# Kernel tuning notes

Measured on AMD Instinct MI355X. Metric: run time of the kernel, lower is better.

Reference implementation:

```python
import jax, jax.numpy as jnp
import numpy as np

NUM_HEADS = 8
KERNEL = 7  # odd, dilation = 1


def _neighbor_indices(n, k):
    # NATTEN semantics: window start clamped so the kxk window stays inside [0, n)
    r = k // 2
    starts = jnp.clip(jnp.arange(n) - r, 0, n - k)  # [n]
    return starts[:, None] + jnp.arange(k)[None, :]  # [n, k]


def setup_inputs() -> dict:
    key = jax.random.key(0)
    k1, k2, k3, k4 = jax.random.split(key, 4)
    B, H, W, C = 2, 56, 56, 256
    return {
        "x": jax.random.normal(k1, (B, H, W, C), dtype=jnp.float32),
        "w_qk": jax.random.normal(k2, (2 * C, C), dtype=jnp.float32) * 0.02,
        "w_v": jax.random.normal(k3, (C, C), dtype=jnp.float32) * 0.02,
        "w_proj": jax.random.normal(k4, (C, C), dtype=jnp.float32) * 0.02,
        "b_proj": jnp.zeros((C,), dtype=jnp.float32),
    }


def reference(x, w_qk, w_v, w_proj, b_proj):
    B, H, W, C = x.shape
    NH, K = NUM_HEADS, KERNEL
    HD = C // NH
    scale = HD ** -0.5

    # qk / v projections (torch Linear: y = x @ W.T)
    qk = (x @ w_qk.T).reshape(B, H, W, 2, NH, HD)
    q = jnp.moveaxis(qk[:, :, :, 0], 3, 1) * scale  # [B, NH, H, W, HD]
    k = jnp.moveaxis(qk[:, :, :, 1], 3, 1)          # [B, NH, H, W, HD]
    v = jnp.moveaxis((x @ w_v.T).reshape(B, H, W, NH, HD), 3, 1)  # [B, NH, H, W, HD]

    idx_h = _neighbor_indices(H, K)  # [H, K]
    idx_w = _neighbor_indices(W, K)  # [W, K]
    ih = idx_h[:, None, :, None]  # [H, 1, K, 1]
    iw = idx_w[None, :, None, :]  # [1, W, 1, K]

    # Gather per-pixel neighborhoods: [B, NH, H, W, K, K, HD]
    k_nb = k[:, :, ih, iw, :]
    v_nb = v[:, :, ih, iw, :]

    # windowed QK^T -> [B, NH, H, W, K*K]
    attn = jnp.einsum('bnijf,bnijpqf->bnijpq', q, k_nb).reshape(B, NH, H, W, K * K)
    attn = jax.nn.softmax(attn, axis=-1)

    # windowed AV -> [B, NH, H, W, HD]
    out = jnp.einsum('bnijk,bnijkf->bnijf', attn, v_nb.reshape(B, NH, H, W, K * K, HD))

    out = jnp.moveaxis(out, 1, 3).reshape(B, H, W, C)
    out = out @ w_proj.T + b_proj
    return out, attn
```

## Files before the change

kernel.cpp:

```cpp
#include <hip/hip_runtime.h>
#include <math.h>

#define Bb   2
#define Hh   56
#define Ww   56
#define Cc   256
#define NHh  8
#define HDd  32
#define KK   7
#define HWsz (Hh*Ww)
#define Mtot (Bb*Hh*Ww)

typedef __bf16 bf16x8 __attribute__((ext_vector_type(8)));
typedef __bf16 bf16x4 __attribute__((ext_vector_type(4)));
typedef float  f32x4  __attribute__((ext_vector_type(4)));

__global__ __launch_bounds__(256) void gemm_qkv(
    const float* __restrict__ A, const float* __restrict__ W0,
    const float* __restrict__ W1, float* __restrict__ OutF,
    __bf16* __restrict__ OutB, float scale)
{
    __shared__ __bf16 As[4096];
    __shared__ __bf16 Bs[4096];

    const int Kdim = 256, n_split = 512;
    const int tid = threadIdx.x;
    const int m0  = blockIdx.y * 64;
    const int n0  = blockIdx.x * 64;

    const int mm = tid >> 2;
    const int q  = tid & 3;
    const float* arow = A + (size_t)(m0 + mm) * Kdim + q * 16;
    const int n_idx = n0 + mm;
    const float* brow = (n_idx < n_split ? W0 + (size_t)n_idx * Kdim
                                         : W1 + (size_t)(n_idx - n_split) * Kdim) + q * 16;

    const int ks_st  = q >> 1;
    const int sub_st = mm >> 4;
    const int row_st = mm & 15;
    const int c0_st  = (q & 1) * 2;
    const int blk_st = ks_st * 4 + sub_st;
    const int off0 = blk_st * 512 + row_st * 32 + ((c0_st ^ (row_st & 3)) * 8);
    const int off1 = blk_st * 512 + row_st * 32 + (((c0_st + 1) ^ (row_st & 3)) * 8);

    const int w    = tid >> 6;
    const int lane = tid & 63;
    const int fr_row = lane & 15;
    const int fr_c   = lane >> 4;
    const int fr_off = fr_row * 32 + ((fr_c ^ (fr_row & 3)) * 8);

    f32x4 acc[4] = {};

    for (int k0 = 0; k0 < Kdim; k0 += 64) {
        float4 a0 = *(const float4*)(arow + k0);
        float4 a1 = *(const float4*)(arow + k0 + 4);
        float4 a2 = *(const float4*)(arow + k0 + 8);
        float4 a3 = *(const float4*)(arow + k0 + 12);
        float4 b0 = *(const float4*)(brow + k0);
        float4 b1 = *(const float4*)(brow + k0 + 4);
        float4 b2 = *(const float4*)(brow + k0 + 8);
        float4 b3 = *(const float4*)(brow + k0 + 12);
        __syncthreads();
        bf16x8 av0 = { (__bf16)a0.x, (__bf16)a0.y, (__bf16)a0.z, (__bf16)a0.w,
                       (__bf16)a1.x, (__bf16)a1.y, (__bf16)a1.z, (__bf16)a1.w };
        bf16x8 av1 = { (__bf16)a2.x, (__bf16)a2.y, (__bf16)a2.z, (__bf16)a2.w,
                       (__bf16)a3.x, (__bf16)a3.y, (__bf16)a3.z, (__bf16)a3.w };
        bf16x8 bv0 = { (__bf16)b0.x, (__bf16)b0.y, (__bf16)b0.z, (__bf16)b0.w,
                       (__bf16)b1.x, (__bf16)b1.y, (__bf16)b1.z, (__bf16)b1.w };
        bf16x8 bv1 = { (__bf16)b2.x, (__bf16)b2.y, (__bf16)b2.z, (__bf16)b2.w,
                       (__bf16)b3.x, (__bf16)b3.y, (__bf16)b3.z, (__bf16)b3.w };
        *(bf16x8*)&As[off0] = av0;
        *(bf16x8*)&As[off1] = av1;
        *(bf16x8*)&Bs[off0] = bv0;
        *(bf16x8*)&Bs[off1] = bv1;
        __syncthreads();
        #pragma unroll
        for (int ks = 0; ks < 2; ++ks) {
            bf16x8 af = *(const bf16x8*)&As[(ks * 4 + w) * 512 + fr_off];
            #pragma unroll
            for (int n = 0; n < 4; ++n) {
                bf16x8 bfr = *(const bf16x8*)&Bs[(ks * 4 + n) * 512 + fr_off];
                acc[n] = __builtin_amdgcn_mfma_f32_16x16x32_bf16(af, bfr, acc[n], 0, 0, 0);
            }
        }
    }

    if (n0 < 256) {
        #pragma unroll
        for (int n = 0; n < 4; ++n) {
            const int gcol = n0 + n * 16 + fr_row;
            #pragma unroll
            for (int r = 0; r < 4; ++r) {
                const int grow = m0 + w * 16 + fr_c * 4 + r;
                OutF[(size_t)grow * 512 + gcol] = acc[n][r] * scale;
            }
        }
    } else {
        #pragma unroll
        for (int n = 0; n < 4; ++n) {
            const int gcol = n0 + n * 16 + fr_row;
            #pragma unroll
            for (int r = 0; r < 4; ++r) {
                const int grow = m0 + w * 16 + fr_c * 4 + r;
                OutB[(size_t)grow * 1024 + 512 + (gcol - 256)] = (__bf16)acc[n][r];
            }
        }
    }
}

__global__ __launch_bounds__(256) void gemm_a16(
    const __bf16* __restrict__ A, const float* __restrict__ W,
    float* __restrict__ Cout, const float* __restrict__ bias)
{
    __shared__ __bf16 As[4096];
    __shared__ __bf16 Bs[4096];

    const int Kdim = 256, N = 256;
    const int tid = threadIdx.x;
    const int m0  = blockIdx.y * 64;
    const int n0  = blockIdx.x * 64;

    const int mm = tid >> 2;
    const int q  = tid & 3;
    const __bf16* arow = A + (size_t)(m0 + mm) * Kdim + q * 16;
    const float*  brow = W + (size_t)(n0 + mm) * Kdim + q * 16;

    const int ks_st  = q >> 1;
    const int sub_st = mm >> 4;
    const int row_st = mm & 15;
    const int c0_st  = (q & 1) * 2;
    const int blk_st = ks_st * 4 + sub_st;
    const int off0 = blk_st * 512 + row_st * 32 + ((c0_st ^ (row_st & 3)) * 8);
    const int off1 = blk_st * 512 + row_st * 32 + (((c0_st + 1) ^ (row_st & 3)) * 8);

    const int w    = tid >> 6;
    const int lane = tid & 63;
    const int fr_row = lane & 15;
    const int fr_c   = lane >> 4;
    const int fr_off = fr_row * 32 + ((fr_c ^ (fr_row & 3)) * 8);

    f32x4 acc[4] = {};

    for (int k0 = 0; k0 < Kdim; k0 += 64) {
        bf16x8 av0 = *(const bf16x8*)(arow + k0);
        bf16x8 av1 = *(const bf16x8*)(arow + k0 + 8);
        float4 b0 = *(const float4*)(brow + k0);
        float4 b1 = *(const float4*)(brow + k0 + 4);
        float4 b2 = *(const float4*)(brow + k0 + 8);
        float4 b3 = *(const float4*)(brow + k0 + 12);
        __syncthreads();
        bf16x8 bv0 = { (__bf16)b0.x, (__bf16)b0.y, (__bf16)b0.z, (__bf16)b0.w,
                       (__bf16)b1.x, (__bf16)b1.y, (__bf16)b1.z, (__bf16)b1.w };
        bf16x8 bv1 = { (__bf16)b2.x, (__bf16)b2.y, (__bf16)b2.z, (__bf16)b2.w,
                       (__bf16)b3.x, (__bf16)b3.y, (__bf16)b3.z, (__bf16)b3.w };
        *(bf16x8*)&As[off0] = av0;
        *(bf16x8*)&As[off1] = av1;
        *(bf16x8*)&Bs[off0] = bv0;
        *(bf16x8*)&Bs[off1] = bv1;
        __syncthreads();
        #pragma unroll
        for (int ks = 0; ks < 2; ++ks) {
            bf16x8 af = *(const bf16x8*)&As[(ks * 4 + w) * 512 + fr_off];
            #pragma unroll
            for (int n = 0; n < 4; ++n) {
                bf16x8 bfr = *(const bf16x8*)&Bs[(ks * 4 + n) * 512 + fr_off];
                acc[n] = __builtin_amdgcn_mfma_f32_16x16x32_bf16(af, bfr, acc[n], 0, 0, 0);
            }
        }
    }

    #pragma unroll
    for (int n = 0; n < 4; ++n) {
        const int gcol = n0 + n * 16 + fr_row;
        const float bs_ = bias[gcol];
        #pragma unroll
        for (int r = 0; r < 4; ++r) {
            const int grow = m0 + w * 16 + fr_c * 4 + r;
            Cout[(size_t)grow * N + gcol] = acc[n][r] + bs_;
        }
    }
}

__global__ __launch_bounds__(256, 5) void nattn_84(
    const float* __restrict__ qkv, __bf16* __restrict__ attn_out,
    float* __restrict__ attn_glob)
{
    __shared__ __align__(16) __bf16 Ks[140 * 40];
    __shared__ float Ss[32 * 49];

    const float*  qf = qkv;
    const __bf16* qb = (const __bf16*)qkv;

    const int bx   = blockIdx.x;
    const int head = bx & 7;
    int t = bx >> 3;
    const int tj = t % 14; t /= 14;
    const int ti = t % 7;
    const int b  = t / 7;
    const int tid = threadIdx.x;

    int base_h = ti * 8 - 3; if (base_h < 0) base_h = 0; if (base_h > Hh - 14) base_h = Hh - 14;
    int base_w = tj * 4 - 3; if (base_w < 0) base_w = 0; if (base_w > Ww - 10) base_w = Ww - 10;

    const int pixb = b * HWsz;
    const int hoff = head * 32;

    #pragma unroll
    for (int it = 0; it < 3; ++it) {
        const int idx = tid + it * 256;
        if (idx < 560) {
            const int p = idx >> 2, c = idx & 3;
            const int pix = pixb + (base_h + p / 10) * Ww + base_w + p % 10;
            *(bf16x8*)&Ks[p * 40 + c * 8] =
                *(const bf16x8*)&qb[(size_t)pix * 1024 + 512 + hoff + c * 8];
        }
    }

    const int q  = tid >> 3;
    const int r  = tid & 7;
    const int qi = ti * 8 + (q >> 2);
    const int qj = tj * 4 + (q & 3);

    float qreg[32];
    {
        const float* qp = &qf[(size_t)(pixb + qi * Ww + qj) * 512 + hoff];
        #pragma unroll
        for (int c = 0; c < 8; ++c) {
            float4 qv = *(const float4*)(qp + c * 4);
            qreg[c * 4 + 0] = qv.x; qreg[c * 4 + 1] = qv.y;
            qreg[c * 4 + 2] = qv.z; qreg[c * 4 + 3] = qv.w;
        }
    }

    bf16x8 vreg[3];
    #pragma unroll
    for (int it = 0; it < 3; ++it) {
        const int idx = tid + it * 256;
        if (idx < 560) {
            const int p = idx >> 2, c = idx & 3;
            const int pix = pixb + (base_h + p / 10) * Ww + base_w + p % 10;
            vreg[it] = *(const bf16x8*)&qb[(size_t)pix * 1024 + 768 + hoff + c * 8];
        }
    }
    __syncthreads();

    int ih0 = qi - 3; if (ih0 < 0) ih0 = 0; if (ih0 > Hh - 7) ih0 = Hh - 7;
    int iw0 = qj - 3; if (iw0 < 0) iw0 = 0; if (iw0 > Ww - 7) iw0 = Ww - 7;
    const int lh0 = ih0 - base_h, lw0 = iw0 - base_w;

    float sc[7];
    float mx = -1e30f;
    #pragma unroll
    for (int tt = 0; tt < 7; ++tt) {
        const int k = r + 8 * tt;
        if (k < 49) {
            const int krow = (lh0 + k / 7) * 10 + lw0 + k % 7;
            const __bf16* kp = &Ks[krow * 40];
            float acc = 0.f;
            #pragma unroll
            for (int c = 0; c < 4; ++c) {
                bf16x8 kv = *(const bf16x8*)(kp + c * 8);
                #pragma unroll
                for (int j = 0; j < 8; ++j)
                    acc += qreg[c * 8 + j] * (float)kv[j];
            }
            sc[tt] = acc;
            mx = fmaxf(mx, acc);
        }
    }
    mx = fmaxf(mx, __shfl_xor(mx, 1));
    mx = fmaxf(mx, __shfl_xor(mx, 2));
    mx = fmaxf(mx, __shfl_xor(mx, 4));
    float sum = 0.f;
    #pragma unroll
    for (int tt = 0; tt < 7; ++tt) {
        const int k = r + 8 * tt;
        if (k < 49) { sc[tt] = __expf(sc[tt] - mx); sum += sc[tt]; }
    }
    sum += __shfl_xor(sum, 1);
    sum += __shfl_xor(sum, 2);
    sum += __shfl_xor(sum, 4);
    const float inv = 1.f / sum;
    #pragma unroll
    for (int tt = 0; tt < 7; ++tt) {
        const int k = r + 8 * tt;
        if (k < 49) Ss[q * 49 + k] = sc[tt] * inv;
    }
    __syncthreads();

    #pragma unroll
    for (int it = 0; it < 3; ++it) {
        const int idx = tid + it * 256;
        if (idx < 560) {
            const int p = idx >> 2, c = idx & 3;
            *(bf16x8*)&Ks[p * 40 + c * 8] = vreg[it];
        }
    }
    const size_t agbase = (size_t)(b * NHh + head) * HWsz;
    for (int idx = tid; idx < 32 * 49; idx += 256) {
        const int qq = idx / 49, k = idx - qq * 49;
        attn_glob[(agbase + (ti * 8 + (qq >> 2)) * Ww + tj * 4 + (qq & 3)) * 49 + k]
            = Ss[qq * 49 + k];
    }
    __syncthreads();

    const int rc  = r & 3;
    const int par = r >> 2;
    float a[8] = {};
    #pragma unroll
    for (int tt = 0; tt < 25; ++tt) {
        const int k = par + 2 * tt;
        if (k < 49) {
            const float pr = Ss[q * 49 + k];
            const int vrow = (lh0 + k / 7) * 10 + lw0 + k % 7;
            bf16x8 v8 = *(const bf16x8*)&Ks[vrow * 40 + rc * 8];
            #pragma unroll
            for (int j = 0; j < 8; ++j)
                a[j] += pr * (float)v8[j];
        }
    }
    #pragma unroll
    for (int j = 0; j < 8; ++j) a[j] += __shfl_xor(a[j], 4);

    bf16x4 o = { (__bf16)a[par * 4 + 0], (__bf16)a[par * 4 + 1],
                 (__bf16)a[par * 4 + 2], (__bf16)a[par * 4 + 3] };
    *(bf16x4*)(attn_out + (size_t)(pixb + qi * Ww + qj) * 256 + hoff + rc * 8 + par * 4) = o;
}

extern "C" void kernel_launch(void* const* d_in, const int* in_sizes, int n_in,
                              void* d_out, int out_size, void* d_ws, size_t ws_size,
                              hipStream_t stream)
{
    const float* x      = (const float*)d_in[0];
    const float* w_qk   = (const float*)d_in[1];
    const float* w_v    = (const float*)d_in[2];
    const float* w_proj = (const float*)d_in[3];
    const float* b_proj = (const float*)d_in[4];

    float* out       = (float*)d_out;
    float* attn_glob = out + (size_t)Mtot * Cc;

    float*  qkv_ws  = (float*)d_ws;
    __bf16* attn_ws = (__bf16*)(qkv_ws + (size_t)Mtot * 512);

    const float scale = 0.17677669529663687f;

    gemm_qkv<<<dim3(768 / 64, Mtot / 64), 256, 0, stream>>>(
        x, w_qk, w_v, qkv_ws, (__bf16*)qkv_ws, scale);

    nattn_84<<<Bb * 7 * 14 * NHh, 256, 0, stream>>>(qkv_ws, attn_ws, attn_glob);

    gemm_a16<<<dim3(256 / 64, Mtot / 64), 256, 0, stream>>>(
        attn_ws, w_proj, out, b_proj);
}
```

Measured before the change: 109.1 us.

## Pre-convert inputs and weights to bf16 and store q in bf16

```diff
diff --git a/kernel.cpp b/kernel.cpp
--- a/kernel.cpp
+++ b/kernel.cpp
@@ -15,25 +15,41 @@
 typedef __bf16 bf16x4 __attribute__((ext_vector_type(4)));
 typedef float  f32x4  __attribute__((ext_vector_type(4)));
 
-__global__ __launch_bounds__(256) void gemm_qkv(
-    const float* __restrict__ A, const float* __restrict__ W0,
-    const float* __restrict__ W1, float* __restrict__ OutF,
-    __bf16* __restrict__ OutB, float scale)
+__global__ __launch_bounds__(256) void prep_bf16(
+    const float* __restrict__ x, const float* __restrict__ wqk,
+    const float* __restrict__ wv, const float* __restrict__ wp,
+    __bf16* __restrict__ xb, __bf16* __restrict__ wallb, __bf16* __restrict__ wpb)
+{
+    const int t = blockIdx.x * 256 + threadIdx.x;
+    const float* src; __bf16* dst; int off;
+    if (t < 200704)      { src = x;   dst = xb;             off = t; }
+    else if (t < 217088) { src = wqk; dst = wallb;          off = t - 200704; }
+    else if (t < 225280) { src = wv;  dst = wallb + 131072; off = t - 217088; }
+    else                 { src = wp;  dst = wpb;            off = t - 225280; }
+    const int e = off * 8;
+    float4 a = *(const float4*)(src + e);
+    float4 b = *(const float4*)(src + e + 4);
+    bf16x8 o = { (__bf16)a.x, (__bf16)a.y, (__bf16)a.z, (__bf16)a.w,
+                 (__bf16)b.x, (__bf16)b.y, (__bf16)b.z, (__bf16)b.w };
+    *(bf16x8*)(dst + e) = o;
+}
+
+__global__ __launch_bounds__(256) void gemm_qkv_b(
+    const __bf16* __restrict__ A, const __bf16* __restrict__ Wall,
+    __bf16* __restrict__ Out, float scale)
 {
     __shared__ __bf16 As[4096];
     __shared__ __bf16 Bs[4096];
 
-    const int Kdim = 256, n_split = 512;
+    const int Kdim = 256;
     const int tid = threadIdx.x;
     const int m0  = blockIdx.y * 64;
     const int n0  = blockIdx.x * 64;
 
     const int mm = tid >> 2;
     const int q  = tid & 3;
-    const float* arow = A + (size_t)(m0 + mm) * Kdim + q * 16;
-    const int n_idx = n0 + mm;
-    const float* brow = (n_idx < n_split ? W0 + (size_t)n_idx * Kdim
-                                         : W1 + (size_t)(n_idx - n_split) * Kdim) + q * 16;
+    const __bf16* arow = A    + (size_t)(m0 + mm) * Kdim + q * 16;
+    const __bf16* brow = Wall + (size_t)(n0 + mm) * Kdim + q * 16;
 
     const int ks_st  = q >> 1;
     const int sub_st = mm >> 4;
@@ -52,23 +68,11 @@
     f32x4 acc[4] = {};
 
     for (int k0 = 0; k0 < Kdim; k0 += 64) {
-        float4 a0 = *(const float4*)(arow + k0);
-        float4 a1 = *(const float4*)(arow + k0 + 4);
-        float4 a2 = *(const float4*)(arow + k0 + 8);
-        float4 a3 = *(const float4*)(arow + k0 + 12);
-        float4 b0 = *(const float4*)(brow + k0);
-        float4 b1 = *(const float4*)(brow + k0 + 4);
-        float4 b2 = *(const float4*)(brow + k0 + 8);
-        float4 b3 = *(const float4*)(brow + k0 + 12);
+        bf16x8 av0 = *(const bf16x8*)(arow + k0);
+        bf16x8 av1 = *(const bf16x8*)(arow + k0 + 8);
+        bf16x8 bv0 = *(const bf16x8*)(brow + k0);
+        bf16x8 bv1 = *(const bf16x8*)(brow + k0 + 8);
         __syncthreads();
-        bf16x8 av0 = { (__bf16)a0.x, (__bf16)a0.y, (__bf16)a0.z, (__bf16)a0.w,
-                       (__bf16)a1.x, (__bf16)a1.y, (__bf16)a1.z, (__bf16)a1.w };
-        bf16x8 av1 = { (__bf16)a2.x, (__bf16)a2.y, (__bf16)a2.z, (__bf16)a2.w,
-                       (__bf16)a3.x, (__bf16)a3.y, (__bf16)a3.z, (__bf16)a3.w };
-        bf16x8 bv0 = { (__bf16)b0.x, (__bf16)b0.y, (__bf16)b0.z, (__bf16)b0.w,
-                       (__bf16)b1.x, (__bf16)b1.y, (__bf16)b1.z, (__bf16)b1.w };
-        bf16x8 bv1 = { (__bf16)b2.x, (__bf16)b2.y, (__bf16)b2.z, (__bf16)b2.w,
-                       (__bf16)b3.x, (__bf16)b3.y, (__bf16)b3.z, (__bf16)b3.w };
         *(bf16x8*)&As[off0] = av0;
         *(bf16x8*)&As[off1] = av1;
         *(bf16x8*)&Bs[off0] = bv0;
@@ -85,31 +89,20 @@
         }
     }
 
-    if (n0 < 256) {
-        #pragma unroll
-        for (int n = 0; n < 4; ++n) {
-            const int gcol = n0 + n * 16 + fr_row;
-            #pragma unroll
-            for (int r = 0; r < 4; ++r) {
-                const int grow = m0 + w * 16 + fr_c * 4 + r;
-                OutF[(size_t)grow * 512 + gcol] = acc[n][r] * scale;
-            }
-        }
-    } else {
-        #pragma unroll
-        for (int n = 0; n < 4; ++n) {
-            const int gcol = n0 + n * 16 + fr_row;
-            #pragma unroll
-            for (int r = 0; r < 4; ++r) {
-                const int grow = m0 + w * 16 + fr_c * 4 + r;
-                OutB[(size_t)grow * 1024 + 512 + (gcol - 256)] = (__bf16)acc[n][r];
-            }
-        }
-    }
-}
-
-__global__ __launch_bounds__(256) void gemm_a16(
-    const __bf16* __restrict__ A, const float* __restrict__ W,
+    #pragma unroll
+    for (int n = 0; n < 4; ++n) {
+        const int gcol = n0 + n * 16 + fr_row;
+        const float sc_ = (gcol < 256) ? scale : 1.f;
+        #pragma unroll
+        for (int r = 0; r < 4; ++r) {
+            const int grow = m0 + w * 16 + fr_c * 4 + r;
+            Out[(size_t)grow * 768 + gcol] = (__bf16)(acc[n][r] * sc_);
+        }
+    }
+}
+
+__global__ __launch_bounds__(256) void gemm_proj_b(
+    const __bf16* __restrict__ A, const __bf16* __restrict__ W,
     float* __restrict__ Cout, const float* __restrict__ bias)
 {
     __shared__ __bf16 As[4096];
@@ -123,7 +116,7 @@
     const int mm = tid >> 2;
     const int q  = tid & 3;
     const __bf16* arow = A + (size_t)(m0 + mm) * Kdim + q * 16;
-    const float*  brow = W + (size_t)(n0 + mm) * Kdim + q * 16;
+    const __bf16* brow = W + (size_t)(n0 + mm) * Kdim + q * 16;
 
     const int ks_st  = q >> 1;
     const int sub_st = mm >> 4;
@@ -144,15 +137,9 @@
     for (int k0 = 0; k0 < Kdim; k0 += 64) {
         bf16x8 av0 = *(const bf16x8*)(arow + k0);
         bf16x8 av1 = *(const bf16x8*)(arow + k0 + 8);
-        float4 b0 = *(const float4*)(brow + k0);
-        float4 b1 = *(const float4*)(brow + k0 + 4);
-        float4 b2 = *(const float4*)(brow + k0 + 8);
-        float4 b3 = *(const float4*)(brow + k0 + 12);
+        bf16x8 bv0 = *(const bf16x8*)(brow + k0);
+        bf16x8 bv1 = *(const bf16x8*)(brow + k0 + 8);
         __syncthreads();
-        bf16x8 bv0 = { (__bf16)b0.x, (__bf16)b0.y, (__bf16)b0.z, (__bf16)b0.w,
-                       (__bf16)b1.x, (__bf16)b1.y, (__bf16)b1.z, (__bf16)b1.w };
-        bf16x8 bv1 = { (__bf16)b2.x, (__bf16)b2.y, (__bf16)b2.z, (__bf16)b2.w,
-                       (__bf16)b3.x, (__bf16)b3.y, (__bf16)b3.z, (__bf16)b3.w };
         *(bf16x8*)&As[off0] = av0;
         *(bf16x8*)&As[off1] = av1;
         *(bf16x8*)&Bs[off0] = bv0;
@@ -182,14 +169,11 @@
 }
 
 __global__ __launch_bounds__(256, 5) void nattn_84(
-    const float* __restrict__ qkv, __bf16* __restrict__ attn_out,
+    const __bf16* __restrict__ qkv, __bf16* __restrict__ attn_out,
     float* __restrict__ attn_glob)
 {
     __shared__ __align__(16) __bf16 Ks[140 * 40];
     __shared__ float Ss[32 * 49];
-
-    const float*  qf = qkv;
-    const __bf16* qb = (const __bf16*)qkv;
 
     const int bx   = blockIdx.x;
     const int head = bx & 7;
@@ -212,7 +196,7 @@
             const int p = idx >> 2, c = idx & 3;
             const int pix = pixb + (base_h + p / 10) * Ww + base_w + p % 10;
             *(bf16x8*)&Ks[p * 40 + c * 8] =
-                *(const bf16x8*)&qb[(size_t)pix * 1024 + 512 + hoff + c * 8];
+                *(const bf16x8*)&qkv[(size_t)pix * 768 + 256 + hoff + c * 8];
         }
     }
 
@@ -223,12 +207,12 @@
 
     float qreg[32];
     {
-        const float* qp = &qf[(size_t)(pixb + qi * Ww + qj) * 512 + hoff];
-        #pragma unroll
-        for (int c = 0; c < 8; ++c) {
-            float4 qv = *(const float4*)(qp + c * 4);
-            qreg[c * 4 + 0] = qv.x; qreg[c * 4 + 1] = qv.y;
-            qreg[c * 4 + 2] = qv.z; qreg[c * 4 + 3] = qv.w;
+        const __bf16* qp = &qkv[(size_t)(pixb + qi * Ww + qj) * 768 + hoff];
+        #pragma unroll
+        for (int c = 0; c < 4; ++c) {
+            bf16x8 qv = *(const bf16x8*)(qp + c * 8);
+            #pragma unroll
+            for (int j = 0; j < 8; ++j) qreg[c * 8 + j] = (float)qv[j];
         }
     }
 
@@ -239,7 +223,7 @@
         if (idx < 560) {
             const int p = idx >> 2, c = idx & 3;
             const int pix = pixb + (base_h + p / 10) * Ww + base_w + p % 10;
-            vreg[it] = *(const bf16x8*)&qb[(size_t)pix * 1024 + 768 + hoff + c * 8];
+            vreg[it] = *(const bf16x8*)&qkv[(size_t)pix * 768 + 512 + hoff + c * 8];
         }
     }
     __syncthreads();
@@ -340,16 +324,21 @@
     float* out       = (float*)d_out;
     float* attn_glob = out + (size_t)Mtot * Cc;
 
-    float*  qkv_ws  = (float*)d_ws;
-    __bf16* attn_ws = (__bf16*)(qkv_ws + (size_t)Mtot * 512);
+    __bf16* xb      = (__bf16*)d_ws;
+    __bf16* wallb   = xb + (size_t)Mtot * 256;
+    __bf16* wpb     = wallb + 768 * 256;
+    __bf16* qkv_ws  = wpb + 256 * 256;
+    __bf16* attn_ws = qkv_ws + (size_t)Mtot * 768;
 
     const float scale = 0.17677669529663687f;
 
-    gemm_qkv<<<dim3(768 / 64, Mtot / 64), 256, 0, stream>>>(
-        x, w_qk, w_v, qkv_ws, (__bf16*)qkv_ws, scale);
+    prep_bf16<<<912, 256, 0, stream>>>(x, w_qk, w_v, w_proj, xb, wallb, wpb);
+
+    gemm_qkv_b<<<dim3(768 / 64, Mtot / 64), 256, 0, stream>>>(
+        xb, wallb, qkv_ws, scale);
 
     nattn_84<<<Bb * 7 * 14 * NHh, 256, 0, stream>>>(qkv_ws, attn_ws, attn_glob);
 
-    gemm_a16<<<dim3(256 / 64, Mtot / 64), 256, 0, stream>>>(
-        attn_ws, w_proj, out, b_proj);
-}
+    gemm_proj_b<<<dim3(256 / 64, Mtot / 64), 256, 0, stream>>>(
+        attn_ws, wpb, out, b_proj);
+}
```

After: 102.7 us. 5.9% less time.
